# Optimization experiments

Measured on AMD Instinct MI355X. Metric: run time of the kernel, lower is better.

## Reference

```python
import jax, jax.numpy as jnp
import numpy as np

B, T, D, H, TW = 4, 4096, 2560, 10, 4
C_CONST = 8.0  # RG-LRU 'c' constant from the paper/code


def setup_inputs() -> dict:
    key = jax.random.key(0)
    ks = jax.random.split(key, 8)
    s = 1.0 / np.sqrt(D)  # variance_scaling fan_in
    Dh = D // H
    return dict(
        x=jax.random.normal(ks[0], (B, T, D), jnp.float32),
        segment_pos=jnp.tile(jnp.arange(T, dtype=jnp.int32), (B, 1)),
        Wy=(jax.random.normal(ks[1], (D, D), jnp.float32) * s),
        by=jnp.zeros((D,), jnp.float32),
        Wx=(jax.random.normal(ks[2], (D, D), jnp.float32) * s),
        bx=jnp.zeros((D,), jnp.float32),
        conv_w=(jax.random.normal(ks[3], (TW, D), jnp.float32) * (1.0 / np.sqrt(TW))),
        conv_b=jnp.zeros((D,), jnp.float32),
        a_param=jax.random.uniform(ks[4], (D,), jnp.float32, minval=-4.0, maxval=-3.0),
        ig_w=(jax.random.normal(ks[5], (H, Dh, Dh), jnp.float32) * (1.0 / np.sqrt(Dh))),
        ig_b=jnp.zeros((H, Dh), jnp.float32),
        ag_w=(jax.random.normal(ks[6], (H, Dh, Dh), jnp.float32) * (1.0 / np.sqrt(Dh))),
        ag_b=jnp.zeros((H, Dh), jnp.float32),
        Wo=(jax.random.normal(ks[7], (D, D), jnp.float32) * s),
        bo=jnp.zeros((D,), jnp.float32),
    )


def _block_diag_linear(x, w, b):
    # x: [B,T,D]; w: [H,Dh,Dh]; b: [H,Dh]
    Bb, Tt, Dd = x.shape
    Hh = w.shape[0]
    xh = x.reshape(Bb, Tt, Hh, -1)
    yh = jnp.einsum('bthd,hdk->bthk', xh, w) + b
    return yh.reshape(Bb, Tt, Dd)


def _forward(x, segment_pos, Wy, by, Wx, bx, conv_w, conv_b, a_param,
             ig_w, ig_b, ag_w, ag_b, Wo, bo):
    # Gate branch: dense + gelu
    y = jax.nn.gelu(x @ Wy + by)
    # Main branch: dense
    xb = x @ Wx + bx
    # Causal depthwise conv1d (left zero pad), w[TW-1] multiplies current token
    tw = conv_w.shape[0]
    seq = xb.shape[1]
    xp = jnp.pad(xb, ((0, 0), (tw - 1, 0), (0, 0)))
    conv = conv_b[None, None]
    for i in range(tw):
        conv = conv + conv_w[i][None, None] * xp[:, i:i + seq]
    # RG-LRU
    reset = (segment_pos == 0)[..., None]  # [B,T,1]
    gate_x = jax.nn.sigmoid(_block_diag_linear(conv, ig_w, ig_b))
    gate_a = jax.nn.sigmoid(_block_diag_linear(conv, ag_w, ag_b))
    log_a = -C_CONST * gate_a * jax.nn.softplus(a_param)  # [B,T,D]
    a = jnp.exp(log_a)
    multiplier = jnp.sqrt(1.0 - jnp.exp(2.0 * log_a))
    multiplier = jnp.where(reset, 1.0, multiplier)
    norm_x = conv * gate_x * multiplier
    a = jnp.where(reset, 0.0, a)
    # diagonal linear scan: h_t = a_t * h_{t-1} + norm_x_t
    def step(h, inp):
        a_t, x_t = inp
        h = a_t * h + x_t
        return h, h
    h0 = jnp.zeros((x.shape[0], a.shape[-1]), a.dtype)
    _, hs = jax.lax.scan(step, h0, (jnp.swapaxes(a, 0, 1), jnp.swapaxes(norm_x, 0, 1)))
    h = jnp.swapaxes(hs, 0, 1)  # [B,T,D]
    # elementwise gate and output projection
    return (h * y) @ Wo + bo


def reference(x, segment_pos, Wy, by, Wx, bx, conv_w, conv_b, a_param,
              ig_w, ig_b, ag_w, ag_b, Wo, bo):
    return _forward(x, segment_pos, Wy, by, Wx, bx, conv_w, conv_b, a_param,
                    ig_w, ig_b, ag_w, ag_b, Wo, bo)
```

## Files before the change

kernel.cpp:

```cpp
#include <hip/hip_runtime.h>

#define D_DIM 2560
#define T_DIM 4096
#define B_DIM 4
#define H_DIM 10
#define DH 256
#define TW_DIM 4
#define M_DIM (B_DIM * T_DIM)
#define CHUNKS 64
#define TC (T_DIM / CHUNKS)

typedef _Float16 f16;
typedef __attribute__((ext_vector_type(8))) _Float16 f16x8;
typedef __attribute__((ext_vector_type(4))) _Float16 f16x4;
typedef __attribute__((ext_vector_type(2))) _Float16 f16x2;
typedef __attribute__((ext_vector_type(4))) float f32x4;
typedef __attribute__((ext_vector_type(2))) float f32x2;

__global__ void cvt_f16_kernel(const float* __restrict__ in, f16* __restrict__ out, long n4) {
  long i = (long)blockIdx.x * blockDim.x + threadIdx.x;
  if (i >= n4) return;
  f32x4 v = ((const f32x4*)in)[i];
  f16x4 o;
  o[0] = (f16)v[0]; o[1] = (f16)v[1]; o[2] = (f16)v[2]; o[3] = (f16)v[3];
  ((f16x4*)out)[i] = o;
}

__global__ void transpose_cvt3_kernel(const float* __restrict__ s0, const float* __restrict__ s1,
                                      const float* __restrict__ s2, f16* __restrict__ out,
                                      int R, int C) {
  __shared__ float tile[32][33];
  const int z = blockIdx.z;
  const float* in = (z == 0) ? s0 : ((z == 1) ? s1 : s2);
  out += (long)z * R * C;
  int c0 = blockIdx.x * 32, r0 = blockIdx.y * 32;
  int tx = threadIdx.x, ty = threadIdx.y;
  for (int i = ty; i < 32; i += 8)
    tile[i][tx] = in[(long)(r0 + i) * C + (c0 + tx)];
  __syncthreads();
  for (int i = ty; i < 32; i += 8)
    out[(long)(c0 + i) * R + (r0 + tx)] = (f16)tile[tx][i];
}

__global__ void transpose_cvt2_kernel(const float* __restrict__ sa, const float* __restrict__ sb,
                                      f16* __restrict__ out, int R, int C, int half) {
  __shared__ float tile[32][33];
  const int z = blockIdx.z;
  const float* in = (z < half) ? (sa + (long)z * R * C) : (sb + (long)(z - half) * R * C);
  out += (long)z * R * C;
  int c0 = blockIdx.x * 32, r0 = blockIdx.y * 32;
  int tx = threadIdx.x, ty = threadIdx.y;
  for (int i = ty; i < 32; i += 8)
    tile[i][tx] = in[(long)(r0 + i) * C + (c0 + tx)];
  __syncthreads();
  for (int i = ty; i < 32; i += 8)
    out[(long)(c0 + i) * R + (r0 + tx)] = (f16)tile[tx][i];
}

__device__ __forceinline__ void async_cp16(const void* g, void* l) {
  __builtin_amdgcn_global_load_lds(
      (const __attribute__((address_space(1))) unsigned int*)g,
      (__attribute__((address_space(3))) unsigned int*)l, 16, 0, 0);
}

__device__ __forceinline__ float fast_sigmoid(float v) {
  return 1.f / (1.f + __expf(-v));
}

#define BM2 256
#define BN2 256

template<int ACT, int OUT16>
__global__ __launch_bounds__(512, 2)
void gemm256_kernel(const f16* __restrict__ A, long ldA,
                    const f16* __restrict__ Bt, long ldB,
                    const float* __restrict__ bias,
                    void* __restrict__ Cv, long ldC, int K) {
  __shared__ __attribute__((aligned(16))) f16 smh[65536];
  const int tid = threadIdx.x;
  const int wave = tid >> 6;
  const int lane = tid & 63;
  const int wm = wave >> 2;
  const int wn = wave & 3;

  const int nx_ = gridDim.x;
  const int nwg = nx_ * gridDim.y;
  int lid = blockIdx.y * nx_ + blockIdx.x;
  lid = (lid & 7) * (nwg >> 3) + (lid >> 3);
  const long bm = (long)(lid / nx_) * BM2;
  const long bn = (long)(lid % nx_) * BN2;

  const int rsub = lane >> 3;
  const int gc8 = (((lane & 7) ^ rsub) & 7) * 8;
  const f16* gA0 = A + (bm + wave * 16 + rsub) * ldA + gc8;
  const f16* gB0 = Bt + (bn + wave * 16 + rsub) * ldB + gc8;
  const int wls = wave * 1024;

#define STG_A(buf, al, ko) do { \
  async_cp16(gA0 + ((al) * 128) * ldA + (ko), smh + (buf) * 32768 + (al) * 8192 + wls); \
  async_cp16(gA0 + ((al) * 128 + 8) * ldA + (ko), smh + (buf) * 32768 + (al) * 8192 + wls + 512); \
} while (0)
#define STG_B(buf, bl, ko) do { \
  async_cp16(gB0 + ((bl) * 128) * ldB + (ko), smh + (buf) * 32768 + 16384 + (bl) * 8192 + wls); \
  async_cp16(gB0 + ((bl) * 128 + 8) * ldB + (ko), smh + (buf) * 32768 + 16384 + (bl) * 8192 + wls + 512); \
} while (0)

  const int quad = lane >> 4, l16 = lane & 15;
  const int sw0 = ((quad ^ (l16 & 7)) & 7) * 8;
  const int sw1 = (((4 + quad) ^ (l16 & 7)) & 7) * 8;
  const int aRB0 = wm * 8192 + l16 * 64;
  const int aRB1 = 32768 + aRB0;
  const int bRB0 = 16384 + (wn >> 1) * 8192 + ((wn & 1) * 64 + l16) * 64;
  const int bRB1 = 32768 + bRB0;

  f16x8 aF[4][2], bF[4][2];
  f32x4 acc[8][4];
#pragma unroll
  for (int i = 0; i < 8; ++i)
#pragma unroll
    for (int j = 0; j < 4; ++j) {
      acc[i][j][0] = 0.f; acc[i][j][1] = 0.f; acc[i][j][2] = 0.f; acc[i][j][3] = 0.f;
    }

#define RD_AQ(base, off) do { _Pragma("unroll") for (int m_ = 0; m_ < 4; ++m_) { \
  aF[m_][0] = *(const f16x8*)&smh[(base) + (off) + m_ * 1024 + sw0]; \
  aF[m_][1] = *(const f16x8*)&smh[(base) + (off) + m_ * 1024 + sw1]; } } while (0)
#define RD_B2(base, n0) do { _Pragma("unroll") for (int n_ = 0; n_ < 2; ++n_) { \
  bF[(n0) + n_][0] = *(const f16x8*)&smh[(base) + ((n0) + n_) * 1024 + sw0]; \
  bF[(n0) + n_][1] = *(const f16x8*)&smh[(base) + ((n0) + n_) * 1024 + sw1]; } } while (0)
#define MMQ(m0, n0) do { _Pragma("unroll") for (int m_ = 0; m_ < 4; ++m_) \
  _Pragma("unroll") for (int n_ = 0; n_ < 2; ++n_) \
    acc[(m0) + m_][(n0) + n_] = __builtin_amdgcn_mfma_f32_16x16x32_f16(aF[m_][1], bF[(n0) + n_][1], \
      __builtin_amdgcn_mfma_f32_16x16x32_f16(aF[m_][0], bF[(n0) + n_][0], acc[(m0) + m_][(n0) + n_], 0, 0, 0), 0, 0, 0); \
} while (0)
#define PH_MID() \
  __builtin_amdgcn_s_barrier(); \
  asm volatile("s_waitcnt lgkmcnt(0)" ::: "memory"); \
  __builtin_amdgcn_sched_barrier(0); \
  __builtin_amdgcn_s_setprio(1)
#define PH_END() \
  __builtin_amdgcn_s_setprio(0); \
  __builtin_amdgcn_s_barrier(); \
  __builtin_amdgcn_sched_barrier(0)
#define PH_END_VM() \
  __builtin_amdgcn_s_setprio(0); \
  asm volatile("s_waitcnt vmcnt(4)" ::: "memory"); \
  __builtin_amdgcn_s_barrier(); \
  __builtin_amdgcn_sched_barrier(0)

  STG_A(1, 0, 64); STG_A(1, 1, 64);
  STG_B(0, 0, 0);  STG_B(0, 1, 0);
  STG_A(0, 0, 0);  STG_A(0, 1, 0);
  STG_B(1, 0, 64); STG_B(1, 1, 64);
  asm volatile("s_waitcnt vmcnt(4)" ::: "memory");
  __builtin_amdgcn_s_barrier();
  __builtin_amdgcn_sched_barrier(0);

  const int NIT = K / 128;
  const int NTm1 = (K / 64) - 1;
#pragma unroll 1
  for (int it = 0; it < NIT; ++it) {
    const long k1 = (long)(2 * it + 1) * 64;
    const long k2 = (long)(2 * it + 2 <= NTm1 ? 2 * it + 2 : NTm1) * 64;
    const long k3 = (long)(2 * it + 3 <= NTm1 ? 2 * it + 3 : NTm1) * 64;
    RD_AQ(aRB0, 0); RD_B2(bRB0, 0); STG_A(1, 0, k1); PH_MID(); MMQ(0, 0); PH_END();
    RD_B2(bRB0, 2); STG_A(1, 1, k1); PH_MID(); MMQ(0, 2); PH_END();
    RD_AQ(aRB0, 4096); STG_B(0, 0, k2); PH_MID(); MMQ(4, 2); PH_END();
    STG_B(0, 1, k2); PH_MID(); MMQ(4, 0); PH_END_VM();
    RD_AQ(aRB1, 0); RD_B2(bRB1, 0); STG_A(0, 0, k2); PH_MID(); MMQ(0, 0); PH_END();
    RD_B2(bRB1, 2); STG_A(0, 1, k2); PH_MID(); MMQ(0, 2); PH_END();
    RD_AQ(aRB1, 4096); STG_B(1, 0, k3); PH_MID(); MMQ(4, 2); PH_END();
    STG_B(1, 1, k3); PH_MID(); MMQ(4, 0); PH_END_VM();
  }
  asm volatile("s_waitcnt vmcnt(0)" ::: "memory");

#pragma unroll
  for (int i = 0; i < 8; ++i) {
    const long row0 = bm + wm * 128 + i * 16 + quad * 4;
#pragma unroll
    for (int j = 0; j < 4; ++j) {
      const long colIn = bn + wn * 64 + j * 16 + l16;
      const float bv = bias[colIn];
#pragma unroll
      for (int r = 0; r < 4; ++r) {
        const long row = row0 + r;
        float v = acc[i][j][r] + bv;
        if (ACT == 1) {
          const float u = v;
          const float tt = 0.7978845608028654f * (u + 0.044715f * u * u * u);
          v = u * fast_sigmoid(2.f * tt);
        }
        const long cidx = row * ldC + colIn;
        if (OUT16) ((f16*)Cv)[cidx] = (f16)v;
        else       ((float*)Cv)[cidx] = v;
      }
    }
  }
#undef STG_A
#undef STG_B
#undef RD_AQ
#undef RD_B2
#undef MMQ
#undef PH_MID
#undef PH_END
#undef PH_END_VM
}

#define BM 128
#define BN 128
#define BK 32

__global__ __launch_bounds__(256, 2)
void gemm_gates_kernel(const f16* __restrict__ A, long ldA,
                       const f16* __restrict__ igt, const f16* __restrict__ agt,
                       const float* __restrict__ igb, const float* __restrict__ agb,
                       const float* __restrict__ apar, const int* __restrict__ segp,
                       f16* __restrict__ aOut, f16* __restrict__ nxOut, int K) {
  __shared__ __attribute__((aligned(16))) f16 As[BM * BK];
  __shared__ __attribute__((aligned(16))) f16 B1s[BN * BK];
  __shared__ __attribute__((aligned(16))) f16 B2s[BN * BK];
  const int tid = threadIdx.x;
  const int wave = tid >> 6;
  const int lane = tid & 63;
  const int wm = wave >> 1, wn = wave & 1;
  const long bm = (long)blockIdx.y * BM;
  const long bn = (long)blockIdx.x * BN;
  const int z = blockIdx.z;
  const f16* Az = A + (long)z * DH;
  const f16* B1 = igt + (long)z * DH * DH;
  const f16* B2 = agt + (long)z * DH * DH;
  const float* b1 = igb + (long)z * DH;
  const float* b2 = agb + (long)z * DH;
  const long cColOff = (long)z * DH;

  const int sRow = wave * 32 + (lane >> 2);
  const int sCol = ((lane & 3) ^ (sRow & 3) ^ ((sRow >> 2) & 3)) * 8;
  const f16* gA = Az + (bm + sRow) * ldA + sCol;
  const f16* gB1 = B1 + (bn + sRow) * (long)K + sCol;
  const f16* gB2 = B2 + (bn + sRow) * (long)K + sCol;
  f16* lA = As + wave * 1024;
  f16* lB1 = B1s + wave * 1024;
  f16* lB2 = B2s + wave * 1024;

  f32x4 accI[4][4], accA[4][4];
#pragma unroll
  for (int i = 0; i < 4; ++i)
#pragma unroll
    for (int j = 0; j < 4; ++j) {
      accI[i][j][0] = 0.f; accI[i][j][1] = 0.f; accI[i][j][2] = 0.f; accI[i][j][3] = 0.f;
      accA[i][j][0] = 0.f; accA[i][j][1] = 0.f; accA[i][j][2] = 0.f; accA[i][j][3] = 0.f;
    }

  const int quad = lane >> 4, l16 = lane & 15;
  const int rswz = (quad ^ (l16 & 3) ^ ((l16 >> 2) & 3)) * 8;

  for (int k0 = 0; k0 < K; k0 += BK) {
    async_cp16(gA, lA);
    async_cp16(gA + 16 * ldA, lA + 512);
    async_cp16(gB1, lB1);
    async_cp16(gB1 + 16 * (long)K, lB1 + 512);
    async_cp16(gB2, lB2);
    async_cp16(gB2 + 16 * (long)K, lB2 + 512);
    gA += BK; gB1 += BK; gB2 += BK;
    __syncthreads();
    f16x8 af[4], bf1[4], bf2[4];
#pragma unroll
    for (int i = 0; i < 4; ++i) {
      af[i]  = *(const f16x8*)&As[(wm * 64 + i * 16 + l16) * BK + rswz];
      bf1[i] = *(const f16x8*)&B1s[(wn * 64 + i * 16 + l16) * BK + rswz];
      bf2[i] = *(const f16x8*)&B2s[(wn * 64 + i * 16 + l16) * BK + rswz];
    }
#pragma unroll
    for (int i = 0; i < 4; ++i)
#pragma unroll
      for (int j = 0; j < 4; ++j) {
        accI[i][j] = __builtin_amdgcn_mfma_f32_16x16x32_f16(af[i], bf1[j], accI[i][j], 0, 0, 0);
        accA[i][j] = __builtin_amdgcn_mfma_f32_16x16x32_f16(af[i], bf2[j], accA[i][j], 0, 0, 0);
      }
    __syncthreads();
  }

#pragma unroll
  for (int i = 0; i < 4; ++i) {
    const long row0 = bm + wm * 64 + i * 16 + quad * 4;
#pragma unroll
    for (int j = 0; j < 4; ++j) {
      const long colIn = bn + wn * 64 + j * 16 + l16;
      const long colG = cColOff + colIn;
      const float bv1 = b1[colIn];
      const float bv2 = b2[colIn];
      const float sp = log1pf(__expf(apar[colG]));
#pragma unroll
      for (int r = 0; r < 4; ++r) {
        const long row = row0 + r;
        const float gx = fast_sigmoid(accI[i][j][r] + bv1);
        const float ga = fast_sigmoid(accA[i][j][r] + bv2);
        const float log_a = -8.f * ga * sp;
        float a = __expf(log_a);
        float mult = sqrtf(fmaxf(1.f - __expf(2.f * log_a), 0.f));
        if (segp[row] == 0) { a = 0.f; mult = 1.f; }
        const long cidx = row * D_DIM + colG;
        const float cv = (float)A[row * ldA + colG];
        aOut[cidx] = (f16)a;
        nxOut[cidx] = (f16)(cv * gx * mult);
      }
    }
  }
}

__global__ void conv_kernel(const f16* __restrict__ xb, const float* __restrict__ cw,
                            const float* __restrict__ cb, f16* __restrict__ out) {
  const int d4 = blockIdx.x * 128 + threadIdx.x;
  const int t = blockIdx.y;
  const int b = blockIdx.z;
  const long idx4 = ((long)b * T_DIM + t) * (D_DIM / 4) + d4;
  f32x4 acc = ((const f32x4*)cb)[d4];
#pragma unroll
  for (int i = 0; i < TW_DIM; ++i) {
    const int tt = t - (TW_DIM - 1) + i;
    if (tt >= 0) {
      f16x4 xv = ((const f16x4*)xb)[idx4 + (long)(i - (TW_DIM - 1)) * (D_DIM / 4)];
      f32x4 w = ((const f32x4*)cw)[i * (D_DIM / 4) + d4];
      acc[0] += w[0] * (float)xv[0];
      acc[1] += w[1] * (float)xv[1];
      acc[2] += w[2] * (float)xv[2];
      acc[3] += w[3] * (float)xv[3];
    }
  }
  f16x4 o;
  o[0] = (f16)acc[0]; o[1] = (f16)acc[1]; o[2] = (f16)acc[2]; o[3] = (f16)acc[3];
  ((f16x4*)out)[idx4] = o;
}

__global__ void scanA_kernel(const f16* __restrict__ a16, const f16* __restrict__ nx16,
                             float* __restrict__ Ac, float* __restrict__ Sc) {
  const int d2 = blockIdx.x * 256 + threadIdx.x;
  const int c = blockIdx.y;
  const int b = blockIdx.z;
  long base2 = ((long)b * T_DIM + (long)c * TC) * (D_DIM / 2) + d2;
  float Ap0 = 1.f, Ap1 = 1.f, S0 = 0.f, S1 = 0.f;
  for (int t = 0; t < TC; ++t) {
    f16x2 av = ((const f16x2*)a16)[base2];
    f16x2 xv = ((const f16x2*)nx16)[base2];
    S0 = (float)av[0] * S0 + (float)xv[0];
    S1 = (float)av[1] * S1 + (float)xv[1];
    Ap0 *= (float)av[0];
    Ap1 *= (float)av[1];
    base2 += D_DIM / 2;
  }
  const long cidx2 = ((long)b * CHUNKS + c) * (D_DIM / 2) + d2;
  f32x2 av_; av_[0] = Ap0; av_[1] = Ap1;
  f32x2 sv_; sv_[0] = S0; sv_[1] = S1;
  ((f32x2*)Ac)[cidx2] = av_;
  ((f32x2*)Sc)[cidx2] = sv_;
}

__global__ void scanB_kernel(const float* __restrict__ Ac, const float* __restrict__ Sc,
                             float* __restrict__ He) {
  const int d = blockIdx.x * 256 + threadIdx.x;
  const int b = blockIdx.z;
  float h = 0.f;
  for (int c = 0; c < CHUNKS; ++c) {
    const long cidx = ((long)b * CHUNKS + c) * D_DIM + d;
    He[cidx] = h;
    h = Ac[cidx] * h + Sc[cidx];
  }
}

__global__ void scanC_kernel(const f16* __restrict__ a16, const f16* __restrict__ nx16,
                             const float* __restrict__ He, const f16* __restrict__ y16,
                             f16* __restrict__ hy16) {
  const int d2 = blockIdx.x * 256 + threadIdx.x;
  const int c = blockIdx.y;
  const int b = blockIdx.z;
  long base2 = ((long)b * T_DIM + (long)c * TC) * (D_DIM / 2) + d2;
  f32x2 hv = ((const f32x2*)He)[((long)b * CHUNKS + c) * (D_DIM / 2) + d2];
  float h0 = hv[0], h1 = hv[1];
  for (int t = 0; t < TC; ++t) {
    f16x2 av = ((const f16x2*)a16)[base2];
    f16x2 xv = ((const f16x2*)nx16)[base2];
    f16x2 yv = ((const f16x2*)y16)[base2];
    h0 = (float)av[0] * h0 + (float)xv[0];
    h1 = (float)av[1] * h1 + (float)xv[1];
    f16x2 o;
    o[0] = (f16)(h0 * (float)yv[0]);
    o[1] = (f16)(h1 * (float)yv[1]);
    ((f16x2*)hy16)[base2] = o;
    base2 += D_DIM / 2;
  }
}

extern "C" void kernel_launch(void* const* d_in, const int* in_sizes, int n_in,
                              void* d_out, int out_size, void* d_ws, size_t ws_size,
                              hipStream_t stream) {
  const float* x   = (const float*)d_in[0];
  const int*   segp= (const int*)d_in[1];
  const float* Wy  = (const float*)d_in[2];
  const float* by  = (const float*)d_in[3];
  const float* Wx  = (const float*)d_in[4];
  const float* bx  = (const float*)d_in[5];
  const float* cw  = (const float*)d_in[6];
  const float* cb  = (const float*)d_in[7];
  const float* ap  = (const float*)d_in[8];
  const float* igw = (const float*)d_in[9];
  const float* igb = (const float*)d_in[10];
  const float* agw = (const float*)d_in[11];
  const float* agb = (const float*)d_in[12];
  const float* Wo  = (const float*)d_in[13];
  const float* bo  = (const float*)d_in[14];
  float* out = (float*)d_out;
  char* ws = (char*)d_ws;

  const long MD = (long)M_DIM * D_DIM;
  f16*   x16    = (f16*)(ws + 0);
  f16*   a16    = (f16*)(ws + 0);
  f16*   y16    = (f16*)(ws + MD * 2);
  f16*   xb2    = (f16*)(ws + MD * 4);
  f16*   hy16   = (f16*)(ws + MD * 4);
  f16*   conv16 = (f16*)(ws + MD * 6);
  f16*   nx16   = (f16*)(ws + MD * 8);
  long off = MD * 10;
  f16* Wt  = (f16*)(ws + off); off += 3L * D_DIM * D_DIM * 2;
  f16* igagt = (f16*)(ws + off); off += 20L * DH * DH * 2;
  float* Ac = (float*)(ws + off); off += (long)B_DIM * CHUNKS * D_DIM * 4;
  float* Sc = (float*)(ws + off); off += (long)B_DIM * CHUNKS * D_DIM * 4;
  float* He = (float*)(ws + off); off += (long)B_DIM * CHUNKS * D_DIM * 4;
  f16* Wyt = Wt;
  f16* Wxt = Wt + (long)D_DIM * D_DIM;
  f16* Wot = Wt + 2L * D_DIM * D_DIM;
  f16* igt = igagt;
  f16* agt = igagt + 10L * DH * DH;

  dim3 tb(32, 8);
  cvt_f16_kernel<<<dim3((unsigned)(MD / 4 / 256)), 256, 0, stream>>>(x, x16, MD / 4);
  transpose_cvt3_kernel<<<dim3(80, 80, 3), tb, 0, stream>>>(Wy, Wx, Wo, Wt, D_DIM, D_DIM);
  transpose_cvt2_kernel<<<dim3(8, 8, 20), tb, 0, stream>>>(igw, agw, igagt, DH, DH, 10);
  gemm256_kernel<1, 1><<<dim3(10, 64, 1), 512, 0, stream>>>(
      x16, D_DIM, Wyt, D_DIM, by, (void*)y16, D_DIM, D_DIM);
  gemm256_kernel<0, 1><<<dim3(10, 64, 1), 512, 0, stream>>>(
      x16, D_DIM, Wxt, D_DIM, bx, (void*)xb2, D_DIM, D_DIM);
  conv_kernel<<<dim3(5, 4096, 4), 128, 0, stream>>>(xb2, cw, cb, conv16);
  gemm_gates_kernel<<<dim3(2, 128, 10), 256, 0, stream>>>(
      conv16, D_DIM, igt, agt, igb, agb, ap, segp, a16, nx16, DH);
  scanA_kernel<<<dim3(5, CHUNKS, 4), 256, 0, stream>>>(a16, nx16, Ac, Sc);
  scanB_kernel<<<dim3(10, 1, 4), 256, 0, stream>>>(Ac, Sc, He);
  scanC_kernel<<<dim3(5, CHUNKS, 4), 256, 0, stream>>>(a16, nx16, He, y16, hy16);
  gemm256_kernel<0, 0><<<dim3(10, 64, 1), 512, 0, stream>>>(
      hy16, D_DIM, Wot, D_DIM, bo, (void*)out, D_DIM, D_DIM);
}
```

Before: 1.344 ms.

## Fuse Wy and Wx GEMMs into one launch and restructure k-loop pipeline

```diff
diff --git a/kernel.cpp b/kernel.cpp
--- a/kernel.cpp
+++ b/kernel.cpp
@@ -70,12 +70,13 @@
 #define BM2 256
 #define BN2 256
 
-template<int ACT, int OUT16>
+template<int FUSED, int OUT16>
 __global__ __launch_bounds__(512, 2)
 void gemm256_kernel(const f16* __restrict__ A, long ldA,
                     const f16* __restrict__ Bt, long ldB,
-                    const float* __restrict__ bias,
-                    void* __restrict__ Cv, long ldC, int K) {
+                    const float* __restrict__ bias0, const float* __restrict__ bias1,
+                    void* __restrict__ C0, void* __restrict__ C1,
+                    long ldC, int K) {
   __shared__ __attribute__((aligned(16))) f16 smh[65536];
   const int tid = threadIdx.x;
   const int wave = tid >> 6;
@@ -108,12 +109,8 @@
   const int quad = lane >> 4, l16 = lane & 15;
   const int sw0 = ((quad ^ (l16 & 7)) & 7) * 8;
   const int sw1 = (((4 + quad) ^ (l16 & 7)) & 7) * 8;
-  const int aRB0 = wm * 8192 + l16 * 64;
-  const int aRB1 = 32768 + aRB0;
-  const int bRB0 = 16384 + (wn >> 1) * 8192 + ((wn & 1) * 64 + l16) * 64;
-  const int bRB1 = 32768 + bRB0;
-
-  f16x8 aF[4][2], bF[4][2];
+
+  f16x8 aL[4][2], aH[4][2], bF[4][2];
   f32x4 acc[8][4];
 #pragma unroll
   for (int i = 0; i < 8; ++i)
@@ -122,88 +119,104 @@
       acc[i][j][0] = 0.f; acc[i][j][1] = 0.f; acc[i][j][2] = 0.f; acc[i][j][3] = 0.f;
     }
 
-#define RD_AQ(base, off) do { _Pragma("unroll") for (int m_ = 0; m_ < 4; ++m_) { \
-  aF[m_][0] = *(const f16x8*)&smh[(base) + (off) + m_ * 1024 + sw0]; \
-  aF[m_][1] = *(const f16x8*)&smh[(base) + (off) + m_ * 1024 + sw1]; } } while (0)
-#define RD_B2(base, n0) do { _Pragma("unroll") for (int n_ = 0; n_ < 2; ++n_) { \
-  bF[(n0) + n_][0] = *(const f16x8*)&smh[(base) + ((n0) + n_) * 1024 + sw0]; \
-  bF[(n0) + n_][1] = *(const f16x8*)&smh[(base) + ((n0) + n_) * 1024 + sw1]; } } while (0)
-#define MMQ(m0, n0) do { _Pragma("unroll") for (int m_ = 0; m_ < 4; ++m_) \
+#define LD8(off) (*(const f16x8*)&smh[(off)])
+#define MM(AX, MB, N0) do { _Pragma("unroll") for (int m_ = 0; m_ < 4; ++m_) \
   _Pragma("unroll") for (int n_ = 0; n_ < 2; ++n_) \
-    acc[(m0) + m_][(n0) + n_] = __builtin_amdgcn_mfma_f32_16x16x32_f16(aF[m_][1], bF[(n0) + n_][1], \
-      __builtin_amdgcn_mfma_f32_16x16x32_f16(aF[m_][0], bF[(n0) + n_][0], acc[(m0) + m_][(n0) + n_], 0, 0, 0), 0, 0, 0); \
+    acc[(MB) + m_][(N0) + n_] = __builtin_amdgcn_mfma_f32_16x16x32_f16(AX[m_][1], bF[(N0) + n_][1], \
+      __builtin_amdgcn_mfma_f32_16x16x32_f16(AX[m_][0], bF[(N0) + n_][0], acc[(MB) + m_][(N0) + n_], 0, 0, 0), 0, 0, 0); \
 } while (0)
-#define PH_MID() \
-  __builtin_amdgcn_s_barrier(); \
+
+#define KSTEP(BUF, S) do { \
+  const long kn_ = (long)((S) + 1 < NT ? (S) + 1 : (S)) * 64; \
+  const int aB_ = (BUF) * 32768 + wm * 8192 + l16 * 64; \
+  const int bB_ = (BUF) * 32768 + 16384 + (wn >> 1) * 8192 + ((wn & 1) * 64 + l16) * 64; \
+  STG_A(BUF ^ 1, 0, kn_); STG_A(BUF ^ 1, 1, kn_); \
+  _Pragma("unroll") for (int m_ = 0; m_ < 4; ++m_) { \
+    aL[m_][0] = LD8(aB_ + m_ * 1024 + sw0); aL[m_][1] = LD8(aB_ + m_ * 1024 + sw1); } \
+  _Pragma("unroll") for (int n_ = 0; n_ < 2; ++n_) { \
+    bF[n_][0] = LD8(bB_ + n_ * 1024 + sw0); bF[n_][1] = LD8(bB_ + n_ * 1024 + sw1); } \
+  STG_B(BUF ^ 1, 0, kn_); \
   asm volatile("s_waitcnt lgkmcnt(0)" ::: "memory"); \
   __builtin_amdgcn_sched_barrier(0); \
-  __builtin_amdgcn_s_setprio(1)
-#define PH_END() \
+  __builtin_amdgcn_s_setprio(1); \
+  MM(aL, 0, 0); \
   __builtin_amdgcn_s_setprio(0); \
+  _Pragma("unroll") for (int n_ = 2; n_ < 4; ++n_) { \
+    bF[n_][0] = LD8(bB_ + n_ * 1024 + sw0); bF[n_][1] = LD8(bB_ + n_ * 1024 + sw1); } \
+  _Pragma("unroll") for (int m_ = 0; m_ < 4; ++m_) { \
+    aH[m_][0] = LD8(aB_ + 4096 + m_ * 1024 + sw0); aH[m_][1] = LD8(aB_ + 4096 + m_ * 1024 + sw1); } \
+  STG_B(BUF ^ 1, 1, kn_); \
+  asm volatile("s_waitcnt lgkmcnt(8)" ::: "memory"); \
+  __builtin_amdgcn_sched_barrier(0); \
+  __builtin_amdgcn_s_setprio(1); \
+  MM(aL, 0, 2); \
+  __builtin_amdgcn_s_setprio(0); \
+  asm volatile("s_waitcnt lgkmcnt(0)" ::: "memory"); \
+  __builtin_amdgcn_sched_barrier(0); \
+  __builtin_amdgcn_s_setprio(1); \
+  MM(aH, 4, 2); MM(aH, 4, 0); \
+  __builtin_amdgcn_s_setprio(0); \
+  asm volatile("s_waitcnt vmcnt(0)" ::: "memory"); \
   __builtin_amdgcn_s_barrier(); \
-  __builtin_amdgcn_sched_barrier(0)
-#define PH_END_VM() \
-  __builtin_amdgcn_s_setprio(0); \
-  asm volatile("s_waitcnt vmcnt(4)" ::: "memory"); \
-  __builtin_amdgcn_s_barrier(); \
-  __builtin_amdgcn_sched_barrier(0)
-
-  STG_A(1, 0, 64); STG_A(1, 1, 64);
-  STG_B(0, 0, 0);  STG_B(0, 1, 0);
-  STG_A(0, 0, 0);  STG_A(0, 1, 0);
-  STG_B(1, 0, 64); STG_B(1, 1, 64);
-  asm volatile("s_waitcnt vmcnt(4)" ::: "memory");
+  __builtin_amdgcn_sched_barrier(0); \
+} while (0)
+
+  const int NT = K / 64;
+
+  STG_A(0, 0, 0); STG_A(0, 1, 0); STG_B(0, 0, 0); STG_B(0, 1, 0);
+  asm volatile("s_waitcnt vmcnt(0)" ::: "memory");
   __builtin_amdgcn_s_barrier();
   __builtin_amdgcn_sched_barrier(0);
 
-  const int NIT = K / 128;
-  const int NTm1 = (K / 64) - 1;
 #pragma unroll 1
-  for (int it = 0; it < NIT; ++it) {
-    const long k1 = (long)(2 * it + 1) * 64;
-    const long k2 = (long)(2 * it + 2 <= NTm1 ? 2 * it + 2 : NTm1) * 64;
-    const long k3 = (long)(2 * it + 3 <= NTm1 ? 2 * it + 3 : NTm1) * 64;
-    RD_AQ(aRB0, 0); RD_B2(bRB0, 0); STG_A(1, 0, k1); PH_MID(); MMQ(0, 0); PH_END();
-    RD_B2(bRB0, 2); STG_A(1, 1, k1); PH_MID(); MMQ(0, 2); PH_END();
-    RD_AQ(aRB0, 4096); STG_B(0, 0, k2); PH_MID(); MMQ(4, 2); PH_END();
-    STG_B(0, 1, k2); PH_MID(); MMQ(4, 0); PH_END_VM();
-    RD_AQ(aRB1, 0); RD_B2(bRB1, 0); STG_A(0, 0, k2); PH_MID(); MMQ(0, 0); PH_END();
-    RD_B2(bRB1, 2); STG_A(0, 1, k2); PH_MID(); MMQ(0, 2); PH_END();
-    RD_AQ(aRB1, 4096); STG_B(1, 0, k3); PH_MID(); MMQ(4, 2); PH_END();
-    STG_B(1, 1, k3); PH_MID(); MMQ(4, 0); PH_END_VM();
-  }
-  asm volatile("s_waitcnt vmcnt(0)" ::: "memory");
-
+  for (int s2 = 0; s2 < NT; s2 += 2) {
+    KSTEP(0, s2);
+    KSTEP(1, s2 + 1);
+  }
+
+  const float* bz = bias0;
+  f16* c16 = (f16*)C0;
+  float* c32 = (float*)C0;
+  long cb = bn;
+  bool doGelu = false;
+  if (FUSED) {
+    const bool h2 = (bn >= 2560);
+    bz = h2 ? bias1 : bias0;
+    c16 = h2 ? (f16*)C1 : (f16*)C0;
+    cb = h2 ? bn - 2560 : bn;
+    doGelu = !h2;
+  }
 #pragma unroll
   for (int i = 0; i < 8; ++i) {
     const long row0 = bm + wm * 128 + i * 16 + quad * 4;
 #pragma unroll
     for (int j = 0; j < 4; ++j) {
-      const long colIn = bn + wn * 64 + j * 16 + l16;
-      const float bv = bias[colIn];
+      const long colW = cb + wn * 64 + j * 16 + l16;
+      const float bv = bz[colW];
 #pragma unroll
       for (int r = 0; r < 4; ++r) {
         const long row = row0 + r;
         float v = acc[i][j][r] + bv;
-        if (ACT == 1) {
-          const float u = v;
-          const float tt = 0.7978845608028654f * (u + 0.044715f * u * u * u);
-          v = u * fast_sigmoid(2.f * tt);
+        if (FUSED) {
+          if (doGelu) {
+            const float u = v;
+            const float tt = 0.7978845608028654f * (u + 0.044715f * u * u * u);
+            v = u * fast_sigmoid(2.f * tt);
+          }
+          c16[row * ldC + colW] = (f16)v;
+        } else if (OUT16) {
+          c16[row * ldC + colW] = (f16)v;
+        } else {
+          c32[row * ldC + colW] = v;
         }
-        const long cidx = row * ldC + colIn;
-        if (OUT16) ((f16*)Cv)[cidx] = (f16)v;
-        else       ((float*)Cv)[cidx] = v;
       }
     }
   }
 #undef STG_A
 #undef STG_B
-#undef RD_AQ
-#undef RD_B2
-#undef MMQ
-#undef PH_MID
-#undef PH_END
-#undef PH_END_VM
+#undef LD8
+#undef MM
+#undef KSTEP
 }
 
 #define BM 128
@@ -425,8 +438,6 @@
   float* Ac = (float*)(ws + off); off += (long)B_DIM * CHUNKS * D_DIM * 4;
   float* Sc = (float*)(ws + off); off += (long)B_DIM * CHUNKS * D_DIM * 4;
   float* He = (float*)(ws + off); off += (long)B_DIM * CHUNKS * D_DIM * 4;
-  f16* Wyt = Wt;
-  f16* Wxt = Wt + (long)D_DIM * D_DIM;
   f16* Wot = Wt + 2L * D_DIM * D_DIM;
   f16* igt = igagt;
   f16* agt = igagt + 10L * DH * DH;
@@ -435,10 +446,8 @@
   cvt_f16_kernel<<<dim3((unsigned)(MD / 4 / 256)), 256, 0, stream>>>(x, x16, MD / 4);
   transpose_cvt3_kernel<<<dim3(80, 80, 3), tb, 0, stream>>>(Wy, Wx, Wo, Wt, D_DIM, D_DIM);
   transpose_cvt2_kernel<<<dim3(8, 8, 20), tb, 0, stream>>>(igw, agw, igagt, DH, DH, 10);
-  gemm256_kernel<1, 1><<<dim3(10, 64, 1), 512, 0, stream>>>(
-      x16, D_DIM, Wyt, D_DIM, by, (void*)y16, D_DIM, D_DIM);
-  gemm256_kernel<0, 1><<<dim3(10, 64, 1), 512, 0, stream>>>(
-      x16, D_DIM, Wxt, D_DIM, bx, (void*)xb2, D_DIM, D_DIM);
+  gemm256_kernel<1, 1><<<dim3(20, 64, 1), 512, 0, stream>>>(
+      x16, D_DIM, Wt, D_DIM, by, bx, (void*)y16, (void*)xb2, D_DIM, D_DIM);
   conv_kernel<<<dim3(5, 4096, 4), 128, 0, stream>>>(xb2, cw, cb, conv16);
   gemm_gates_kernel<<<dim3(2, 128, 10), 256, 0, stream>>>(
       conv16, D_DIM, igt, agt, igb, agb, ap, segp, a16, nx16, DH);
@@ -446,5 +455,5 @@
   scanB_kernel<<<dim3(10, 1, 4), 256, 0, stream>>>(Ac, Sc, He);
   scanC_kernel<<<dim3(5, CHUNKS, 4), 256, 0, stream>>>(a16, nx16, He, y16, hy16);
   gemm256_kernel<0, 0><<<dim3(10, 64, 1), 512, 0, stream>>>(
-      hy16, D_DIM, Wot, D_DIM, bo, (void*)out, D_DIM, D_DIM);
-}
+      hy16, D_DIM, Wot, D_DIM, bo, nullptr, (void*)out, nullptr, D_DIM, D_DIM);
+}
```

New measurement: 1.600 ms. +19.1%, slower.

## Restructure GEMM main loop sync with split A fragments and relaxed waits

Applied to the files above, without the earlier changes.

```diff
diff --git a/kernel.cpp b/kernel.cpp
--- a/kernel.cpp
+++ b/kernel.cpp
@@ -113,7 +113,7 @@
   const int bRB0 = 16384 + (wn >> 1) * 8192 + ((wn & 1) * 64 + l16) * 64;
   const int bRB1 = 32768 + bRB0;
 
-  f16x8 aF[4][2], bF[4][2];
+  f16x8 aL[4][2], aH[4][2], bF[4][2];
   f32x4 acc[8][4];
 #pragma unroll
   for (int i = 0; i < 8; ++i)
@@ -122,55 +122,55 @@
       acc[i][j][0] = 0.f; acc[i][j][1] = 0.f; acc[i][j][2] = 0.f; acc[i][j][3] = 0.f;
     }
 
-#define RD_AQ(base, off) do { _Pragma("unroll") for (int m_ = 0; m_ < 4; ++m_) { \
-  aF[m_][0] = *(const f16x8*)&smh[(base) + (off) + m_ * 1024 + sw0]; \
-  aF[m_][1] = *(const f16x8*)&smh[(base) + (off) + m_ * 1024 + sw1]; } } while (0)
+#define LD8(off) (*(const f16x8*)&smh[(off)])
+#define RD_A(AX, base, off) do { _Pragma("unroll") for (int m_ = 0; m_ < 4; ++m_) { \
+  AX[m_][0] = LD8((base) + (off) + m_ * 1024 + sw0); \
+  AX[m_][1] = LD8((base) + (off) + m_ * 1024 + sw1); } } while (0)
 #define RD_B2(base, n0) do { _Pragma("unroll") for (int n_ = 0; n_ < 2; ++n_) { \
-  bF[(n0) + n_][0] = *(const f16x8*)&smh[(base) + ((n0) + n_) * 1024 + sw0]; \
-  bF[(n0) + n_][1] = *(const f16x8*)&smh[(base) + ((n0) + n_) * 1024 + sw1]; } } while (0)
-#define MMQ(m0, n0) do { _Pragma("unroll") for (int m_ = 0; m_ < 4; ++m_) \
+  bF[(n0) + n_][0] = LD8((base) + ((n0) + n_) * 1024 + sw0); \
+  bF[(n0) + n_][1] = LD8((base) + ((n0) + n_) * 1024 + sw1); } } while (0)
+#define MM(AX, MB, N0) do { _Pragma("unroll") for (int m_ = 0; m_ < 4; ++m_) \
   _Pragma("unroll") for (int n_ = 0; n_ < 2; ++n_) \
-    acc[(m0) + m_][(n0) + n_] = __builtin_amdgcn_mfma_f32_16x16x32_f16(aF[m_][1], bF[(n0) + n_][1], \
-      __builtin_amdgcn_mfma_f32_16x16x32_f16(aF[m_][0], bF[(n0) + n_][0], acc[(m0) + m_][(n0) + n_], 0, 0, 0), 0, 0, 0); \
+    acc[(MB) + m_][(N0) + n_] = __builtin_amdgcn_mfma_f32_16x16x32_f16(AX[m_][1], bF[(N0) + n_][1], \
+      __builtin_amdgcn_mfma_f32_16x16x32_f16(AX[m_][0], bF[(N0) + n_][0], acc[(MB) + m_][(N0) + n_], 0, 0, 0), 0, 0, 0); \
 } while (0)
-#define PH_MID() \
-  __builtin_amdgcn_s_barrier(); \
-  asm volatile("s_waitcnt lgkmcnt(0)" ::: "memory"); \
-  __builtin_amdgcn_sched_barrier(0); \
-  __builtin_amdgcn_s_setprio(1)
-#define PH_END() \
-  __builtin_amdgcn_s_setprio(0); \
-  __builtin_amdgcn_s_barrier(); \
-  __builtin_amdgcn_sched_barrier(0)
-#define PH_END_VM() \
-  __builtin_amdgcn_s_setprio(0); \
-  asm volatile("s_waitcnt vmcnt(4)" ::: "memory"); \
-  __builtin_amdgcn_s_barrier(); \
-  __builtin_amdgcn_sched_barrier(0)
-
-  STG_A(1, 0, 64); STG_A(1, 1, 64);
-  STG_B(0, 0, 0);  STG_B(0, 1, 0);
-  STG_A(0, 0, 0);  STG_A(0, 1, 0);
+#define SP1 __builtin_amdgcn_s_setprio(1)
+#define SP0 __builtin_amdgcn_s_setprio(0)
+#define PH_BAR() asm volatile("s_barrier" ::: "memory")
+#define PH_VM6() do { asm volatile("s_waitcnt vmcnt(6)" ::: "memory"); \
+                      asm volatile("s_barrier" ::: "memory"); } while (0)
+
+  const int NT = K / 64;
+  const int NIT = NT / 2;
+
+  STG_A(0, 0, 0); STG_A(0, 1, 0);
+  STG_B(0, 0, 0); STG_B(0, 1, 0);
   STG_B(1, 0, 64); STG_B(1, 1, 64);
   asm volatile("s_waitcnt vmcnt(4)" ::: "memory");
-  __builtin_amdgcn_s_barrier();
-  __builtin_amdgcn_sched_barrier(0);
-
-  const int NIT = K / 128;
-  const int NTm1 = (K / 64) - 1;
+  asm volatile("s_barrier" ::: "memory");
+
 #pragma unroll 1
   for (int it = 0; it < NIT; ++it) {
-    const long k1 = (long)(2 * it + 1) * 64;
-    const long k2 = (long)(2 * it + 2 <= NTm1 ? 2 * it + 2 : NTm1) * 64;
-    const long k3 = (long)(2 * it + 3 <= NTm1 ? 2 * it + 3 : NTm1) * 64;
-    RD_AQ(aRB0, 0); RD_B2(bRB0, 0); STG_A(1, 0, k1); PH_MID(); MMQ(0, 0); PH_END();
-    RD_B2(bRB0, 2); STG_A(1, 1, k1); PH_MID(); MMQ(0, 2); PH_END();
-    RD_AQ(aRB0, 4096); STG_B(0, 0, k2); PH_MID(); MMQ(4, 2); PH_END();
-    STG_B(0, 1, k2); PH_MID(); MMQ(4, 0); PH_END_VM();
-    RD_AQ(aRB1, 0); RD_B2(bRB1, 0); STG_A(0, 0, k2); PH_MID(); MMQ(0, 0); PH_END();
-    RD_B2(bRB1, 2); STG_A(0, 1, k2); PH_MID(); MMQ(0, 2); PH_END();
-    RD_AQ(aRB1, 4096); STG_B(1, 0, k3); PH_MID(); MMQ(4, 2); PH_END();
-    STG_B(1, 1, k3); PH_MID(); MMQ(4, 0); PH_END_VM();
+    const int s = 2 * it;
+    const long k1 = (long)(s + 1) * 64;
+    const long k2 = (long)(s + 2 < NT ? s + 2 : NT - 1) * 64;
+    const long k3 = (long)(s + 3 < NT ? s + 3 : NT - 1) * 64;
+    RD_A(aL, aRB0, 0); RD_B2(bRB0, 0); STG_A(1, 0, k1);
+    SP1; MM(aL, 0, 0); SP0; PH_BAR();
+    RD_B2(bRB0, 2); STG_A(1, 1, k1);
+    SP1; MM(aL, 0, 2); SP0; PH_VM6();
+    RD_A(aH, aRB0, 4096); STG_B(0, 0, k2);
+    SP1; MM(aH, 4, 2); SP0; PH_BAR();
+    STG_B(0, 1, k2);
+    SP1; MM(aH, 4, 0); SP0; PH_VM6();
+    RD_A(aL, aRB1, 0); RD_B2(bRB1, 0); STG_A(0, 0, k2);
+    SP1; MM(aL, 0, 0); SP0; PH_BAR();
+    RD_B2(bRB1, 2); STG_A(0, 1, k2);
+    SP1; MM(aL, 0, 2); SP0; PH_VM6();
+    RD_A(aH, aRB1, 4096); STG_B(1, 0, k3);
+    SP1; MM(aH, 4, 2); SP0; PH_BAR();
+    STG_B(1, 1, k3);
+    SP1; MM(aH, 4, 0); SP0; PH_VM6();
   }
   asm volatile("s_waitcnt vmcnt(0)" ::: "memory");
 
@@ -198,12 +198,14 @@
   }
 #undef STG_A
 #undef STG_B
-#undef RD_AQ
+#undef LD8
+#undef RD_A
 #undef RD_B2
-#undef MMQ
-#undef PH_MID
-#undef PH_END
-#undef PH_END_VM
+#undef MM
+#undef SP1
+#undef SP0
+#undef PH_BAR
+#undef PH_VM6
 }
 
 #define BM 128
```

New measurement: 1.349 ms. Within noise of the previous version (+0.4%).
